# Kernel tuning notes

Measured on AMD Instinct MI355X. Metric: run time of the kernel, lower is better.

## Reference

```python
import math
import numpy as np
import jax, jax.numpy as jnp

LMAX1, LMAX2 = 10, 5
F1, F2 = 20, 40
B_IN, B_L1, B_L2 = 96, 10, 6
ASPECT = 2
BATCH = 32
ACT_CST = math.sqrt(2.0)  # normalize2mom(relu): E[relu(z)^2]=1/2 for z~N(0,1)


def _fact(n):
    return float(math.factorial(n))


def wigner_d_small(l, beta):
    # Wigner small-d matrices, complex-m ordering m=-l..l -> [n, 2l+1, 2l+1]
    beta = np.asarray(beta, dtype=np.float64)
    n = beta.shape[0]
    d = np.zeros((n, 2 * l + 1, 2 * l + 1))
    c, s = np.cos(beta / 2), np.sin(beta / 2)
    for imp, mp in enumerate(range(-l, l + 1)):
        for im, m in enumerate(range(-l, l + 1)):
            pref = math.sqrt(_fact(l + mp) * _fact(l - mp) * _fact(l + m) * _fact(l - m))
            val = np.zeros(n)
            for k in range(max(0, m - mp), min(l + m, l - mp) + 1):
                den = _fact(l + m - k) * _fact(k) * _fact(mp - m + k) * _fact(l - mp - k)
                val += (-1.0) ** (mp - m + k) / den * c ** (2 * l + m - mp - 2 * k) * s ** (mp - m + 2 * k)
            d[:, imp, im] = pref * val
    return d


def U_c2r(l):
    # unitary change of basis complex SH -> real SH, Yr = U @ Yc
    U = np.zeros((2 * l + 1, 2 * l + 1), dtype=np.complex128)
    U[l, l] = 1.0
    sq = 1.0 / math.sqrt(2.0)
    for m in range(1, l + 1):
        cs = (-1.0) ** m
        U[l + m, l + m] = cs * sq
        U[l + m, l - m] = sq
        U[l - m, l + m] = -1j * cs * sq
        U[l - m, l - m] = 1j * sq
    return U


def rot_z_real(l, ang):
    # real-basis rotation about the azimuthal axis -> [n, 2l+1, 2l+1]
    U = U_c2r(l)
    m = np.arange(-l, l + 1)
    ph = np.exp(-1j * np.outer(np.asarray(ang, np.float64), m))
    return np.real(np.einsum('ik,nk,jk->nij', U, ph, U.conj(), optimize=True))


def d_real(l, beta):
    U = U_c2r(l)
    dc = wigner_d_small(l, beta).astype(np.complex128)
    return np.real(np.einsum('ij,njk,lk->nil', U, dc, U.conj(), optimize=True))


def wigner_D_pts(l, a, b, g):
    return np.einsum('nij,njk,nkm->nim', rot_z_real(l, a), d_real(l, b), rot_z_real(l, g), optimize=True)


def flat_wigner_pts(lmax, a, b, g):
    n = len(a)
    return np.concatenate([math.sqrt(2 * l + 1) * wigner_D_pts(l, a, b, g).reshape(n, -1) for l in range(lmax + 1)], -1)


def flat_wigner_grid(lmax, al, be, ga):
    # product grid (alpha x beta x gamma), flattened alpha-major -> [na*nb*ng, sum (2l+1)^2]
    blocks = []
    for l in range(lmax + 1):
        D = np.einsum('aij,bjk,gkm->abgim', rot_z_real(l, al), d_real(l, be), rot_z_real(l, ga), optimize=True)
        blocks.append(math.sqrt(2 * l + 1) * D.reshape(-1, (2 * l + 1) ** 2))
    return np.concatenate(blocks, -1)


def sh_pts(lmax, a, b):
    # component-normalized real SH at points: Y_l = sqrt(2l+1) * D^l(a,b,0)[:, m=0]
    cols = []
    for l in range(lmax + 1):
        M = np.einsum('nij,nj->ni', rot_z_real(l, a), d_real(l, b)[:, :, l], optimize=True)
        cols.append(math.sqrt(2 * l + 1) * M)
    return np.concatenate(cols, -1)


def sh_grid(lmax, al, be):
    # SH on product grid, flattened beta-major to match x.transpose(-1,-2) layout
    cols = []
    for l in range(lmax + 1):
        M = np.einsum('aij,bj->bai', rot_z_real(l, al), d_real(l, be)[:, :, l], optimize=True)
        cols.append(math.sqrt(2 * l + 1) * M.reshape(-1, 2 * l + 1))
    return np.concatenate(cols, -1)


def _so3_grid(res):
    nb, na = 2 * res, 2 * res * ASPECT
    al = 2 * math.pi * np.arange(na) / na
    be = math.pi * (np.arange(nb) + 0.5) / nb
    return al, be, al.copy()


def setup_inputs():
    key = jax.random.key(0)
    k1, k2, k3 = jax.random.split(key, 3)
    # kernel grids (near identity), as in s2/so3_near_identity_grid
    b_s2 = np.arange(1, 4) * (math.pi / 8) / 3
    a_s2 = np.linspace(0, 2 * math.pi, 9)[:-1]
    ga, gb = np.meshgrid(a_s2, b_s2, indexing='ij')
    Yk1 = sh_pts(LMAX1, ga.ravel(), gb.ravel())  # [24, 121]
    a_so3 = np.linspace(0, 2 * math.pi, 8)[:-1]
    g_so3 = np.linspace(-2 * math.pi, 2 * math.pi, 8)
    ga, gb, gg = np.meshgrid(a_so3, b_s2, g_so3, indexing='ij')
    Dk2 = flat_wigner_pts(LMAX2, ga.ravel(), gb.ravel(), gg.ravel())  # [168, 286]
    # FromS2Grid analysis matrix (pinv of band-limited synthesis matrix)
    be = (np.arange(B_IN) + 0.5) / B_IN * math.pi
    al = np.arange(B_IN) / B_IN * 2 * math.pi
    from_s2 = np.linalg.pinv(sh_grid(LMAX1, al, be))  # [121, 9216]
    # SO(3) activation transform matrices
    a1, b1, g1 = _so3_grid(B_L1)
    D1_to = flat_wigner_grid(LMAX1, a1, b1, g1)                     # [32000, 1771]
    F1_from = np.linalg.pinv(flat_wigner_grid(LMAX2, a1, b1, g1))   # [286, 32000]
    a2, b2, g2 = _so3_grid(B_L2)
    D2_to = flat_wigner_grid(LMAX2, a2, b2, g2)                     # [6912, 286]
    F2_from = np.linalg.pinv(flat_wigner_grid(0, a2, b2, g2))       # [1, 6912]
    f32 = lambda v: jnp.asarray(v, dtype=jnp.float32)
    return {
        'x': jax.random.normal(k1, (BATCH, 1, B_IN, B_IN), dtype=jnp.float32),
        'w1': jax.random.normal(k2, (1, F1, Yk1.shape[0]), dtype=jnp.float32),
        'w2': jax.random.normal(k3, (F1, F2, Dk2.shape[0]), dtype=jnp.float32),
        'Yk1': f32(Yk1), 'Dk2': f32(Dk2), 'from_s2': f32(from_s2),
        'D1_to': f32(D1_to), 'F1_from': f32(F1_from),
        'D2_to': f32(D2_to), 'F2_from': f32(F2_from),
    }


def reference(x, w1, w2, Yk1, Dk2, from_s2, D1_to, F1_from, D2_to, F2_from):
    B = x.shape[0]
    # [B,1,alpha,beta] -> [B,1,beta,alpha] -> S2 Fourier coefficients
    c = jnp.einsum('bfg,cg->bfc', jnp.swapaxes(x, -1, -2).reshape(B, 1, -1), from_s2)  # [B,1,121]
    # S2 -> SO(3) convolution (e3nn Linear with SH-built weights)
    psi1 = jnp.einsum('ni,xyn->xyi', Yk1, w1) / math.sqrt(Yk1.shape[0])  # [1,F1,121]
    outs = []
    for l in range(LMAX1 + 1):
        k = 2 * l + 1
        ol = jnp.einsum('bim,ijn->bjnm', c[:, :, l * l:l * l + k], psi1[:, :, l * l:l * l + k])  # fan_in = 1
        outs.append(ol.reshape(B, F1, k * k))
    h = jnp.concatenate(outs, -1)  # [B,F1,1771]
    # SO(3) activation: Fourier -> grid, relu, grid -> Fourier (lmax 10 -> 5)
    g = ACT_CST * jax.nn.relu(jnp.einsum('bfc,gc->bfg', h, D1_to))
    h = jnp.einsum('bfg,cg->bfc', g, F1_from)  # [B,F1,286]
    # SO(3) -> SO(3) convolution (Wigner-D-built weights)
    psi2 = jnp.einsum('nc,xyn->xyc', Dk2, w2) / math.sqrt(Dk2.shape[0])  # [F1,F2,286]
    outs, off = [], 0
    for l in range(LMAX2 + 1):
        k = 2 * l + 1
        xl = h[:, :, off:off + k * k].reshape(B, F1, k, k)       # [B,i,u,m]
        pl = psi2[:, :, off:off + k * k].reshape(F1, F2, k, k)   # [i,j,u,v]
        ol = jnp.einsum('bium,ijuv->bjvm', xl, pl) / math.sqrt(F1 * k)  # fan_in = F1*(2l+1)
        outs.append(ol.reshape(B, F2, k * k))
        off += k * k
    h = jnp.concatenate(outs, -1)  # [B,F2,286]
    # final SO(3) activation lmax 5 -> 0
    g = ACT_CST * jax.nn.relu(jnp.einsum('bfc,gc->bfg', h, D2_to))
    return jnp.einsum('bfg,cg->bfc', g, F2_from)  # [B,F2,1]
```

## Files before the change

kernel.cpp:

```cpp
#include <hip/hip_runtime.h>
#include <hip/hip_bf16.h>
#include <math.h>


#define B_      32
#define F1_     20
#define F2_     40
#define NC1     1771
#define K1P     1792
#define NG1     32000
#define NC2     286
#define K2P     288
#define NG2     6912
#define SQRT2_  1.41421356237309515f
#define RS24    0.20412414523193154f
#define RS168   0.07715167498104595f

typedef unsigned int   uint32;
typedef unsigned short u16;
typedef __attribute__((ext_vector_type(8))) short short8;
typedef __attribute__((ext_vector_type(4))) float f32x4;

#define AS1(p) ((const __attribute__((address_space(1))) void*)(p))
#define AS3(p) ((__attribute__((address_space(3))) void*)(p))

#define WAITCNT_VM4 0x0F74

__device__ __forceinline__ u16 f2bf(float f) {
  uint32 u = __float_as_uint(f);
  return (u16)((u + 0x7FFFu + ((u >> 16) & 1u)) >> 16);
}
__device__ __forceinline__ uint32 pack_bf16(float lo, float hi) {
  uint32 a = __float_as_uint(lo), b = __float_as_uint(hi);
  a = (a + 0x7FFFu + ((a >> 16) & 1u)) >> 16;
  b = (b + 0x7FFFu + ((b >> 16) & 1u)) & 0xFFFF0000u;
  return a | b;
}

__device__ __forceinline__ float wave_reduce(float v) {
#pragma unroll
  for (int o = 32; o > 0; o >>= 1) v += __shfl_down(v, o, 64);
  return v;
}


__global__ void k_xt(const float* __restrict__ x, float* __restrict__ xt) {
  __shared__ float t[32][33];
  const int b = blockIdx.z, i0 = blockIdx.x * 32, j0 = blockIdx.y * 32;
  const int tx = threadIdx.x & 31, ty0 = threadIdx.x >> 5;
  const float* xb = x + b * 9216;
  float* xtb = xt + b * 9216;
#pragma unroll
  for (int r = 0; r < 4; ++r) {
    const int ty = ty0 + r * 8;
    t[ty][tx] = xb[(i0 + ty) * 96 + j0 + tx];
  }
  __syncthreads();
#pragma unroll
  for (int r = 0; r < 4; ++r) {
    const int ty = ty0 + r * 8;
    xtb[(j0 + ty) * 96 + i0 + tx] = t[tx][ty];
  }
}

__global__ void k_c2(const float* __restrict__ xt, const float* __restrict__ fs,
                     float* __restrict__ c) {
  const int ch = blockIdx.x, b = blockIdx.y, tid = threadIdx.x;
  const float4* xb = (const float4*)(xt + b * 9216);
  const float4* fr = (const float4*)(fs + ch * 9216);
  float s = 0.f;
#pragma unroll 3
  for (int g = tid; g < 2304; g += 256) {
    const float4 a = xb[g], d = fr[g];
    s += a.x * d.x + a.y * d.y + a.z * d.z + a.w * d.w;
  }
  s = wave_reduce(s);
  __shared__ float red[4];
  if ((tid & 63) == 0) red[tid >> 6] = s;
  __syncthreads();
  if (tid == 0) c[b * 121 + ch] = red[0] + red[1] + red[2] + red[3];
}

__global__ void k_c(const float* __restrict__ x, const float* __restrict__ fs,
                    float* __restrict__ c) {
  const int ch = blockIdx.x, b = blockIdx.y, tid = threadIdx.x;
  const float* xb = x + b * 9216;
  const float* fr = fs + ch * 9216;
  float s = 0.f;
  for (int g = tid; g < 9216; g += 256) {
    s += xb[(g % 96) * 96 + (g / 96)] * fr[g];
  }
  s = wave_reduce(s);
  __shared__ float red[4];
  if ((tid & 63) == 0) red[tid >> 6] = s;
  __syncthreads();
  if (tid == 0) c[b * 121 + ch] = red[0] + red[1] + red[2] + red[3];
}

__global__ void k_psi1(const float* __restrict__ Yk1, const float* __restrict__ w1,
                       float* __restrict__ psi1) {
  const int j = blockIdx.x, i = threadIdx.x;
  __shared__ float wsm[24];
  if (i < 24) wsm[i] = w1[j * 24 + i];
  __syncthreads();
  if (i < 121) {
    float s = 0.f;
#pragma unroll
    for (int n = 0; n < 24; ++n) s += Yk1[n * 121 + i] * wsm[n];
    psi1[j * 121 + i] = s * RS24;
  }
}

__global__ void k_h(const float* __restrict__ c, const float* __restrict__ psi1,
                    u16* __restrict__ hb) {
  const int j = blockIdx.x, b = blockIdx.y, tid = threadIdx.x;
  __shared__ float cs[121], ps[121];
  if (tid < 121) { cs[tid] = c[b * 121 + tid]; ps[tid] = psi1[j * 121 + tid]; }
  __syncthreads();
  for (int idx = tid; idx < K1P; idx += 256) {
    u16 v = 0;
    if (idx < NC1) {
      int off = 0, l = 0, k = 1;
      while (idx >= off + k * k) { off += k * k; ++l; k += 2; }
      const int r = idx - off, n = r / k, m = r % k;
      v = f2bf(cs[l * l + m] * ps[l * l + n]);
    }
    hb[(size_t)(b * F1_ + j) * K1P + idx] = v;
  }
}


__global__ void k_cvt1(const float* __restrict__ in, uint32* __restrict__ out) {
  const int total = 32000 * 896;
  for (int id = blockIdx.x * 256 + threadIdx.x; id < total; id += gridDim.x * 256) {
    const int r = id / 896, c2 = id % 896, cc = c2 * 2;
    const float* p = in + (size_t)r * NC1 + cc;
    const float lo = (cc < NC1) ? p[0] : 0.f;
    const float hi = (cc + 1 < NC1) ? p[1] : 0.f;
    out[id] = pack_bf16(lo, hi);
  }
}

__global__ void k_cvt2(const float* __restrict__ in, uint32* __restrict__ out) {
  const int total = 286 * 16000;
  for (int id = blockIdx.x * 256 + threadIdx.x; id < total; id += gridDim.x * 256) {
    out[id] = pack_bf16(in[2 * id], in[2 * id + 1]);
  }
}

__global__ void k_cvt3(const float* __restrict__ in, uint32* __restrict__ out) {
  const int total = 6912 * 144;
  for (int id = blockIdx.x * 256 + threadIdx.x; id < total; id += gridDim.x * 256) {
    const int r = id / 144, c2 = id % 144, cc = c2 * 2;
    const float* p = in + (size_t)r * NC2 + cc;
    const float lo = (cc < NC2) ? p[0] : 0.f;
    const float hi = (cc + 1 < NC2) ? p[1] : 0.f;
    out[id] = pack_bf16(lo, hi);
  }
}


__launch_bounds__(256)
__global__ void k_gemm1_v4(const u16* __restrict__ A, const u16* __restrict__ B,
                           u16* __restrict__ C) {
  __shared__ __align__(16) u16 As0[128 * 32], As1[128 * 32], As2[128 * 32];
  __shared__ __align__(16) u16 Bs0[128 * 32], Bs1[128 * 32], Bs2[128 * 32];
  const int bid = blockIdx.x;
  const int gg = bid / 40, loc = bid % 40;
  int nt, mt;
  if (gg < 31) { nt = gg * 8 + (loc & 7); mt = loc >> 3; }
  else         { nt = 248 + (loc & 1);   mt = loc >> 1; }
  const int m0 = mt * 128, n0 = nt * 128;
  const int tid = threadIdx.x;
  const int lane = tid & 63, w = tid >> 6;
  const int wm = w >> 1, wn = w & 1;
  const int q = lane >> 4, r16 = lane & 15;

  const u16* ag = A + (size_t)(m0 + (tid >> 2)) * K1P + (tid & 3) * 8;
  const u16* bg = B + (size_t)(n0 + (tid >> 2)) * K1P + (tid & 3) * 8;

#define G1_ISSUE(kk, Asb, Bsb)                                                   \
  {                                                                              \
    _Pragma("unroll")                                                            \
    for (int i = 0; i < 2; ++i) {                                                \
      __builtin_amdgcn_global_load_lds(AS1(ag + (kk) * 32 + (size_t)i * 64 * K1P), \
          AS3((char*)(Asb) + i * 4096 + w * 1024), 16, 0, 0);                    \
      __builtin_amdgcn_global_load_lds(AS1(bg + (kk) * 32 + (size_t)i * 64 * K1P), \
          AS3((char*)(Bsb) + i * 4096 + w * 1024), 16, 0, 0);                    \
    }                                                                            \
  }

#define G1_COMPUTE(Asb, Bsb)                                                     \
  {                                                                              \
    short8 af[4], bq[4];                                                         \
    _Pragma("unroll")                                                            \
    for (int mb = 0; mb < 4; ++mb)                                               \
      af[mb] = *(const short8*)&(Asb)[(wm * 64 + mb * 16 + r16) * 32 + q * 8];   \
    _Pragma("unroll")                                                            \
    for (int nb = 0; nb < 4; ++nb)                                               \
      bq[nb] = *(const short8*)&(Bsb)[(wn * 64 + nb * 16 + r16) * 32 + q * 8];   \
    _Pragma("unroll")                                                            \
    for (int mb = 0; mb < 4; ++mb)                                               \
      _Pragma("unroll")                                                          \
      for (int nb = 0; nb < 4; ++nb)                                             \
        acc[mb][nb] = __builtin_amdgcn_mfma_f32_16x16x32_bf16(af[mb], bq[nb],    \
                                                              acc[mb][nb], 0, 0, 0); \
  }

#define G1_STAGE(kk, AsR, BsR, AsI, BsI)        \
  {                                             \
    __builtin_amdgcn_s_waitcnt(WAITCNT_VM4);    \
    __builtin_amdgcn_s_barrier();               \
    asm volatile("" ::: "memory");              \
    if ((kk) + 2 < 56) G1_ISSUE((kk) + 2, AsI, BsI) \
    G1_COMPUTE(AsR, BsR)                        \
  }

  f32x4 acc[4][4] = {};
  G1_ISSUE(0, As0, Bs0)
  G1_ISSUE(1, As1, Bs1)
  for (int k = 0; k < 54; k += 3) {
    G1_STAGE(k,     As0, Bs0, As2, Bs2)
    G1_STAGE(k + 1, As1, Bs1, As0, Bs0)
    G1_STAGE(k + 2, As2, Bs2, As1, Bs1)
  }
  G1_STAGE(54, As0, Bs0, As2, Bs2)
  G1_STAGE(55, As1, Bs1, As0, Bs0)

#pragma unroll
  for (int mb = 0; mb < 4; ++mb) {
#pragma unroll
    for (int nb = 0; nb < 4; ++nb) {
      const int col = n0 + wn * 64 + nb * 16 + r16;
#pragma unroll
      for (int r = 0; r < 4; ++r) {
        const int row = m0 + wm * 64 + mb * 16 + q * 4 + r;
        float v = acc[mb][nb][r];
        v = (v > 0.f) ? v * SQRT2_ : 0.f;
        C[(size_t)row * NG1 + col] = f2bf(v);
      }
    }
  }
#undef G1_ISSUE
#undef G1_COMPUTE
#undef G1_STAGE
}

__launch_bounds__(256)
__global__ void k_gemm2_v4(const u16* __restrict__ A, const u16* __restrict__ B,
                           float* __restrict__ C) {
  __shared__ __align__(16) u16 As0[128 * 32], As1[128 * 32], As2[128 * 32];
  __shared__ __align__(16) u16 Bs0[128 * 32], Bs1[128 * 32], Bs2[128 * 32];
  const int m0 = blockIdx.x * 128, n0 = blockIdx.y * 128;
  const int ks = blockIdx.z * 1600;
  const int tid = threadIdx.x;
  const int lane = tid & 63, w = tid >> 6;
  const int wm = w >> 1, wn = w & 1;
  const int q = lane >> 4, r16 = lane & 15;

  const u16* ag = A + (size_t)(m0 + (tid >> 2)) * NG1 + ks + (tid & 3) * 8;
  int rb0 = n0 + (tid >> 2);        if (rb0 > 285) rb0 = 285;
  int rb1 = n0 + (tid >> 2) + 64;   if (rb1 > 285) rb1 = 285;
  const u16* bg0 = B + (size_t)rb0 * NG1 + ks + (tid & 3) * 8;
  const u16* bg1 = B + (size_t)rb1 * NG1 + ks + (tid & 3) * 8;

#define G2_ISSUE(kk, Asb, Bsb)                                                   \
  {                                                                              \
    _Pragma("unroll")                                                            \
    for (int i = 0; i < 2; ++i)                                                  \
      __builtin_amdgcn_global_load_lds(AS1(ag + (kk) * 32 + (size_t)i * 64 * NG1), \
          AS3((char*)(Asb) + i * 4096 + w * 1024), 16, 0, 0);                    \
    __builtin_amdgcn_global_load_lds(AS1(bg0 + (kk) * 32),                       \
        AS3((char*)(Bsb) + w * 1024), 16, 0, 0);                                 \
    __builtin_amdgcn_global_load_lds(AS1(bg1 + (kk) * 32),                       \
        AS3((char*)(Bsb) + 4096 + w * 1024), 16, 0, 0);                          \
  }

#define G2_COMPUTE(Asb, Bsb)                                                     \
  {                                                                              \
    short8 af[4], bq[4];                                                         \
    _Pragma("unroll")                                                            \
    for (int mb = 0; mb < 4; ++mb)                                               \
      af[mb] = *(const short8*)&(Asb)[(wm * 64 + mb * 16 + r16) * 32 + q * 8];   \
    _Pragma("unroll")                                                            \
    for (int nb = 0; nb < 4; ++nb)                                               \
      bq[nb] = *(const short8*)&(Bsb)[(wn * 64 + nb * 16 + r16) * 32 + q * 8];   \
    _Pragma("unroll")                                                            \
    for (int mb = 0; mb < 4; ++mb)                                               \
      _Pragma("unroll")                                                          \
      for (int nb = 0; nb < 4; ++nb)                                             \
        acc[mb][nb] = __builtin_amdgcn_mfma_f32_16x16x32_bf16(af[mb], bq[nb],    \
                                                              acc[mb][nb], 0, 0, 0); \
  }

#define G2_STAGE(kk, AsR, BsR, AsI, BsI)        \
  {                                             \
    __builtin_amdgcn_s_waitcnt(WAITCNT_VM4);    \
    __builtin_amdgcn_s_barrier();               \
    asm volatile("" ::: "memory");              \
    if ((kk) + 2 < 50) G2_ISSUE((kk) + 2, AsI, BsI) \
    G2_COMPUTE(AsR, BsR)                        \
  }

  f32x4 acc[4][4] = {};
  G2_ISSUE(0, As0, Bs0)
  G2_ISSUE(1, As1, Bs1)
  for (int k = 0; k < 48; k += 3) {
    G2_STAGE(k,     As0, Bs0, As2, Bs2)
    G2_STAGE(k + 1, As1, Bs1, As0, Bs0)
    G2_STAGE(k + 2, As2, Bs2, As1, Bs1)
  }
  G2_STAGE(48, As0, Bs0, As2, Bs2)
  G2_STAGE(49, As1, Bs1, As0, Bs0)

#pragma unroll
  for (int mb = 0; mb < 4; ++mb) {
#pragma unroll
    for (int nb = 0; nb < 4; ++nb) {
      const int col = n0 + wn * 64 + nb * 16 + r16;
      if (col < NC2) {
#pragma unroll
        for (int r = 0; r < 4; ++r) {
          const int row = m0 + wm * 64 + mb * 16 + q * 4 + r;
          atomicAdd(&C[(size_t)row * NC2 + col], acc[mb][nb][r]);
        }
      }
    }
  }
#undef G2_ISSUE
#undef G2_COMPUTE
#undef G2_STAGE
}

__launch_bounds__(256)
__global__ void k_gemm3_v3(const u16* __restrict__ A, const u16* __restrict__ B,
                           const float* __restrict__ wv, float* __restrict__ out) {
  __shared__ __align__(16) u16 As[128 * 32];
  __shared__ __align__(16) u16 Bs[128 * 32];
  __shared__ float red[128][33];
  const int m0 = blockIdx.x * 128, n0 = blockIdx.y * 128;
  const int tid = threadIdx.x;
  const int lane = tid & 63, w = tid >> 6;
  const int wm = w >> 1, wn = w & 1;
  const int q = lane >> 4, r16 = lane & 15;

  f32x4 acc[4][4] = {};
  const u16* ag = A + (size_t)(m0 + (tid >> 2)) * K2P + (tid & 3) * 8;
  const u16* bg = B + (size_t)(n0 + (tid >> 2)) * K2P + (tid & 3) * 8;

  for (int k0 = 0; k0 < K2P; k0 += 32) {
#pragma unroll
    for (int i = 0; i < 2; ++i) {
      __builtin_amdgcn_global_load_lds(AS1(ag + k0 + (size_t)i * 64 * K2P),
                                       AS3((char*)As + i * 4096 + w * 1024), 16, 0, 0);
      __builtin_amdgcn_global_load_lds(AS1(bg + k0 + (size_t)i * 64 * K2P),
                                       AS3((char*)Bs + i * 4096 + w * 1024), 16, 0, 0);
    }
    __syncthreads();
    short8 af[4], bq[4];
#pragma unroll
    for (int mb = 0; mb < 4; ++mb)
      af[mb] = *(const short8*)&As[(wm * 64 + mb * 16 + r16) * 32 + q * 8];
#pragma unroll
    for (int nb = 0; nb < 4; ++nb)
      bq[nb] = *(const short8*)&Bs[(wn * 64 + nb * 16 + r16) * 32 + q * 8];
#pragma unroll
    for (int mb = 0; mb < 4; ++mb)
#pragma unroll
      for (int nb = 0; nb < 4; ++nb)
        acc[mb][nb] = __builtin_amdgcn_mfma_f32_16x16x32_bf16(af[mb], bq[nb], acc[mb][nb], 0, 0, 0);
    __syncthreads();
  }
  float wvv[4];
#pragma unroll
  for (int nb = 0; nb < 4; ++nb) wvv[nb] = wv[n0 + wn * 64 + nb * 16 + r16];
#pragma unroll
  for (int mb = 0; mb < 4; ++mb) {
#pragma unroll
    for (int r = 0; r < 4; ++r) {
      const int rowl = wm * 64 + mb * 16 + q * 4 + r;
      float t = 0.f;
#pragma unroll
      for (int nb = 0; nb < 4; ++nb) {
        float v = acc[mb][nb][r];
        v = (v > 0.f) ? v : 0.f;
        t += v * wvv[nb];
      }
      red[rowl][wn * 16 + r16] = t;
    }
  }
  __syncthreads();
  if (tid < 128) {
    float s = 0.f;
#pragma unroll
    for (int cc = 0; cc < 32; ++cc) s += red[tid][cc];
    atomicAdd(&out[m0 + tid], s * SQRT2_);
  }
}


__launch_bounds__(256)
__global__ void k_gemm1_mfma(const u16* __restrict__ A, const float* __restrict__ Bf,
                             u16* __restrict__ C) {
  __shared__ __align__(16) u16 As[128 * 32];
  __shared__ __align__(16) u16 Bs[128 * 32];
  const int tid = threadIdx.x;
  const int lane = tid & 63, w = tid >> 6;
  const int wm = w >> 1, wn = w & 1;
  const int q = lane >> 4, r16 = lane & 15;
  const int m0 = blockIdx.x * 128, n0 = blockIdx.y * 128;

  f32x4 acc[4][4] = {};
  const u16* ag = A + (size_t)(m0 + (tid >> 2)) * K1P + (tid & 3) * 8;

  for (int k0 = 0; k0 < K1P; k0 += 32) {
#pragma unroll
    for (int i = 0; i < 2; ++i) {
      __builtin_amdgcn_global_load_lds(AS1(ag + k0 + (size_t)i * 64 * K1P),
                                       AS3((char*)As + i * 4096 + w * 1024), 16, 0, 0);
    }
#pragma unroll
    for (int i = 0; i < 8; ++i) {
      const int p = i * 256 + tid;
      const int row = p >> 4, c2 = (p & 15) * 2;
      const int kk = k0 + c2;
      const float* bp = Bf + (size_t)(n0 + row) * NC1 + kk;
      const float lo = (kk < NC1) ? bp[0] : 0.f;
      const float hi = (kk + 1 < NC1) ? bp[1] : 0.f;
      ((uint32*)Bs)[row * 16 + (p & 15)] = pack_bf16(lo, hi);
    }
    __syncthreads();
    short8 af[4], bq[4];
#pragma unroll
    for (int mb = 0; mb < 4; ++mb)
      af[mb] = *(const short8*)&As[(wm * 64 + mb * 16 + r16) * 32 + q * 8];
#pragma unroll
    for (int nb = 0; nb < 4; ++nb)
      bq[nb] = *(const short8*)&Bs[(wn * 64 + nb * 16 + r16) * 32 + q * 8];
#pragma unroll
    for (int mb = 0; mb < 4; ++mb)
#pragma unroll
      for (int nb = 0; nb < 4; ++nb)
        acc[mb][nb] = __builtin_amdgcn_mfma_f32_16x16x32_bf16(af[mb], bq[nb], acc[mb][nb], 0, 0, 0);
    __syncthreads();
  }
#pragma unroll
  for (int mb = 0; mb < 4; ++mb) {
#pragma unroll
    for (int nb = 0; nb < 4; ++nb) {
      const int col = n0 + wn * 64 + nb * 16 + r16;
#pragma unroll
      for (int r = 0; r < 4; ++r) {
        const int row = m0 + wm * 64 + mb * 16 + q * 4 + r;
        float v = acc[mb][nb][r];
        v = (v > 0.f) ? v * SQRT2_ : 0.f;
        C[(size_t)row * NG1 + col] = f2bf(v);
      }
    }
  }
}

__launch_bounds__(256)
__global__ void k_gemm2_mfma(const u16* __restrict__ A, const float* __restrict__ Bf,
                             float* __restrict__ C) {
  __shared__ __align__(16) u16 As[128 * 32];
  __shared__ __align__(16) u16 Bs[128 * 32];
  const int tid = threadIdx.x;
  const int lane = tid & 63, w = tid >> 6;
  const int wm = w >> 1, wn = w & 1;
  const int q = lane >> 4, r16 = lane & 15;
  const int m0 = blockIdx.x * 128, n0 = blockIdx.y * 128;
  const int ks = blockIdx.z * 1600;

  f32x4 acc[4][4] = {};
  const u16* ag = A + (size_t)(m0 + (tid >> 2)) * NG1 + ks + (tid & 3) * 8;

  for (int kt = 0; kt < 1600; kt += 32) {
#pragma unroll
    for (int i = 0; i < 2; ++i) {
      __builtin_amdgcn_global_load_lds(AS1(ag + kt + (size_t)i * 64 * NG1),
                                       AS3((char*)As + i * 4096 + w * 1024), 16, 0, 0);
    }
#pragma unroll
    for (int i = 0; i < 4; ++i) {
      const int idx = i * 256 + tid;
      const int row = idx >> 3, c4 = (idx & 7) * 4;
      const int n = n0 + row;
      float4 v = make_float4(0.f, 0.f, 0.f, 0.f);
      if (n < NC2) v = *(const float4*)(Bf + (size_t)n * NG1 + ks + kt + c4);
      ((uint32*)Bs)[row * 16 + (idx & 7) * 2]     = pack_bf16(v.x, v.y);
      ((uint32*)Bs)[row * 16 + (idx & 7) * 2 + 1] = pack_bf16(v.z, v.w);
    }
    __syncthreads();
    short8 af[4], bq[4];
#pragma unroll
    for (int mb = 0; mb < 4; ++mb)
      af[mb] = *(const short8*)&As[(wm * 64 + mb * 16 + r16) * 32 + q * 8];
#pragma unroll
    for (int nb = 0; nb < 4; ++nb)
      bq[nb] = *(const short8*)&Bs[(wn * 64 + nb * 16 + r16) * 32 + q * 8];
#pragma unroll
    for (int mb = 0; mb < 4; ++mb)
#pragma unroll
      for (int nb = 0; nb < 4; ++nb)
        acc[mb][nb] = __builtin_amdgcn_mfma_f32_16x16x32_bf16(af[mb], bq[nb], acc[mb][nb], 0, 0, 0);
    __syncthreads();
  }
#pragma unroll
  for (int mb = 0; mb < 4; ++mb) {
#pragma unroll
    for (int nb = 0; nb < 4; ++nb) {
      const int col = n0 + wn * 64 + nb * 16 + r16;
      if (col < NC2) {
#pragma unroll
        for (int r = 0; r < 4; ++r) {
          const int row = m0 + wm * 64 + mb * 16 + q * 4 + r;
          atomicAdd(&C[(size_t)row * NC2 + col], acc[mb][nb][r]);
        }
      }
    }
  }
}


__global__ void k_psi2(const float* __restrict__ Dk2, const float* __restrict__ w2,
                       float* __restrict__ psi2) {
  const int blk = blockIdx.x, tid = threadIdx.x;
  __shared__ float w2s[168];
  if (tid < 168) w2s[tid] = w2[blk * 168 + tid];
  __syncthreads();
  for (int cc = tid; cc < NC2; cc += 256) {
    float s = 0.f;
    for (int n = 0; n < 168; ++n) s += Dk2[n * NC2 + cc] * w2s[n];
    psi2[blk * NC2 + cc] = s * RS168;
  }
}

__global__ void k_step7(const float* __restrict__ h2, const float* __restrict__ psi2,
                        u16* __restrict__ h3b) {
  const int j = blockIdx.x, b = blockIdx.y, tid = threadIdx.x;
  __shared__ float sh[20 * 286];
  __shared__ float sp[20 * 286];
  for (int e = tid; e < 20 * 286; e += 256) {
    const int i = e / 286, cc = e % 286;
    sh[e] = h2[(b * F1_ + i) * NC2 + cc];
    sp[e] = psi2[(i * F2_ + j) * NC2 + cc];
  }
  __syncthreads();
  for (int cidx = tid; cidx < K2P; cidx += 256) {
    u16 ov = 0;
    if (cidx < NC2) {
      int off = 0, l = 0, k = 1;
      while (cidx >= off + k * k) { off += k * k; ++l; k += 2; }
      const int r = cidx - off, v = r / k, m = r % k;
      float acc = 0.f;
      for (int i = 0; i < 20; ++i) {
        const float* hbp = &sh[i * 286 + off];
        const float* pb = &sp[i * 286 + off];
        for (int u = 0; u < k; ++u) acc += hbp[u * k + m] * pb[u * k + v];
      }
      ov = f2bf(acc * rsqrtf(20.f * (float)k));
    }
    h3b[(size_t)(b * F2_ + j) * K2P + cidx] = ov;
  }
}


extern "C" void kernel_launch(void* const* d_in, const int* in_sizes, int n_in,
                              void* d_out, int out_size, void* d_ws, size_t ws_size,
                              hipStream_t stream) {
  const float* x       = (const float*)d_in[0];
  const float* w1      = (const float*)d_in[1];
  const float* w2      = (const float*)d_in[2];
  const float* Yk1     = (const float*)d_in[3];
  const float* Dk2     = (const float*)d_in[4];
  const float* from_s2 = (const float*)d_in[5];
  const float* D1_to   = (const float*)d_in[6];
  const float* F1_from = (const float*)d_in[7];
  const float* D2_to   = (const float*)d_in[8];
  const float* F2_from = (const float*)d_in[9];
  float* out = (float*)d_out;

  float* ws = (float*)d_ws;
  float* c    = ws + 0;
  float* psi1 = ws + 3872;
  float* h2   = ws + 6292;
  float* psi2 = ws + 189332;
  u16*   h3b  = (u16*)(ws + 418132);
  u16*   hb   = (u16*)(ws + 602452);
  u16*   g    = (u16*)(ws + 1175892);
  u16*   D2bf = (u16*)(ws + 11415892);
  u16*   F1bf = (u16*)(ws + 12411220);
  u16*   D1bf = (u16*)(ws + 16987220);
  float* x_t  = ws + 45659220;
  const size_t BIG_NEED = (size_t)45659220 * 4;
  const size_t XT_NEED  = (size_t)45954132 * 4;
  const bool big   = ws_size >= BIG_NEED;
  const bool useXT = ws_size >= XT_NEED;

  if (useXT) {
    k_xt<<<dim3(3, 3, 32), 256, 0, stream>>>(x, x_t);
    k_c2<<<dim3(121, 32),  256, 0, stream>>>(x_t, from_s2, c);
  } else {
    k_c <<<dim3(121, 32),  256, 0, stream>>>(x, from_s2, c);
  }
  k_psi1<<<dim3(20),      128, 0, stream>>>(Yk1, w1, psi1);
  k_h   <<<dim3(20, 32),  256, 0, stream>>>(c, psi1, hb);
  k_cvt3<<<dim3(1024),    256, 0, stream>>>(D2_to, (uint32*)D2bf);

  if (big) {
    k_cvt1<<<dim3(8192), 256, 0, stream>>>(D1_to, (uint32*)D1bf);
    k_cvt2<<<dim3(4096), 256, 0, stream>>>(F1_from, (uint32*)F1bf);
    k_gemm1_v4<<<dim3(1250), 256, 0, stream>>>(hb, D1bf, g);
    hipMemsetAsync(h2, 0, (size_t)640 * 286 * sizeof(float), stream);
    k_gemm2_v4<<<dim3(5, 3, 20), 256, 0, stream>>>(g, F1bf, h2);
  } else {
    k_gemm1_mfma<<<dim3(5, 250), 256, 0, stream>>>(hb, D1_to, g);
    hipMemsetAsync(h2, 0, (size_t)640 * 286 * sizeof(float), stream);
    k_gemm2_mfma<<<dim3(5, 3, 20), 256, 0, stream>>>(g, F1_from, h2);
  }

  k_psi2 <<<dim3(800),    256, 0, stream>>>(Dk2, w2, psi2);
  k_step7<<<dim3(40, 32), 256, 0, stream>>>(h2, psi2, h3b);

  hipMemsetAsync(out, 0, (size_t)1280 * sizeof(float), stream);
  k_gemm3_v3<<<dim3(10, 54), 256, 0, stream>>>(h3b, D2bf, F2_from, out);
}
```

Measured before the change: 674.8 us.

## Replace LDS-staged GEMM pipelines with direct global-to-register double-buffered MFMA loads

Both large GEMM kernels drop the three-stage LDS ring buffer filled by global_load_lds with barriers. Each wave now loads its MFMA operand fragments straight from global memory into registers, double-buffered across k-chunks, with launch bounds requesting 3 blocks per CU. GEMM2's split-K changes from 20 to 25 slices of 1280. This removes LDS traffic and block-wide barriers but gives up cross-wave reuse through shared memory, so each wave refetches A/B rows from global/L2 with 16-byte strided accesses, raising cache pressure.

```diff
diff --git a/kernel.cpp b/kernel.cpp
--- a/kernel.cpp
+++ b/kernel.cpp
@@ -24,8 +24,6 @@
 #define AS1(p) ((const __attribute__((address_space(1))) void*)(p))
 #define AS3(p) ((__attribute__((address_space(3))) void*)(p))
 
-#define WAITCNT_VM4 0x0F74
-
 __device__ __forceinline__ u16 f2bf(float f) {
   uint32 u = __float_as_uint(f);
   return (u16)((u + 0x7FFFu + ((u >> 16) & 1u)) >> 16);
@@ -160,11 +158,27 @@
 }
 
 
-__launch_bounds__(256)
-__global__ void k_gemm1_v4(const u16* __restrict__ A, const u16* __restrict__ B,
+#define MFMA16(ab, bb)                                                          \
+  {                                                                             \
+    _Pragma("unroll")                                                           \
+    for (int mb = 0; mb < 4; ++mb)                                              \
+      _Pragma("unroll")                                                         \
+      for (int nb = 0; nb < 4; ++nb)                                            \
+        acc[mb][nb] = __builtin_amdgcn_mfma_f32_16x16x32_bf16((ab)[mb], (bb)[nb], \
+                                                              acc[mb][nb], 0, 0, 0); \
+  }
+
+#define LD8(ab, bb, kc)                                                         \
+  {                                                                             \
+    _Pragma("unroll")                                                           \
+    for (int mb = 0; mb < 4; ++mb) (ab)[mb] = *(const short8*)(ap[mb] + (kc) * 32); \
+    _Pragma("unroll")                                                           \
+    for (int nb = 0; nb < 4; ++nb) (bb)[nb] = *(const short8*)(bp[nb] + (kc) * 32); \
+  }
+
+__launch_bounds__(256, 3)
+__global__ void k_gemm1_v5(const u16* __restrict__ A, const u16* __restrict__ B,
                            u16* __restrict__ C) {
-  __shared__ __align__(16) u16 As0[128 * 32], As1[128 * 32], As2[128 * 32];
-  __shared__ __align__(16) u16 Bs0[128 * 32], Bs1[128 * 32], Bs2[128 * 32];
   const int bid = blockIdx.x;
   const int gg = bid / 40, loc = bid % 40;
   int nt, mt;
@@ -176,56 +190,27 @@
   const int wm = w >> 1, wn = w & 1;
   const int q = lane >> 4, r16 = lane & 15;
 
-  const u16* ag = A + (size_t)(m0 + (tid >> 2)) * K1P + (tid & 3) * 8;
-  const u16* bg = B + (size_t)(n0 + (tid >> 2)) * K1P + (tid & 3) * 8;
-
-#define G1_ISSUE(kk, Asb, Bsb)                                                   \
-  {                                                                              \
-    _Pragma("unroll")                                                            \
-    for (int i = 0; i < 2; ++i) {                                                \
-      __builtin_amdgcn_global_load_lds(AS1(ag + (kk) * 32 + (size_t)i * 64 * K1P), \
-          AS3((char*)(Asb) + i * 4096 + w * 1024), 16, 0, 0);                    \
-      __builtin_amdgcn_global_load_lds(AS1(bg + (kk) * 32 + (size_t)i * 64 * K1P), \
-          AS3((char*)(Bsb) + i * 4096 + w * 1024), 16, 0, 0);                    \
-    }                                                                            \
-  }
-
-#define G1_COMPUTE(Asb, Bsb)                                                     \
-  {                                                                              \
-    short8 af[4], bq[4];                                                         \
-    _Pragma("unroll")                                                            \
-    for (int mb = 0; mb < 4; ++mb)                                               \
-      af[mb] = *(const short8*)&(Asb)[(wm * 64 + mb * 16 + r16) * 32 + q * 8];   \
-    _Pragma("unroll")                                                            \
-    for (int nb = 0; nb < 4; ++nb)                                               \
-      bq[nb] = *(const short8*)&(Bsb)[(wn * 64 + nb * 16 + r16) * 32 + q * 8];   \
-    _Pragma("unroll")                                                            \
-    for (int mb = 0; mb < 4; ++mb)                                               \
-      _Pragma("unroll")                                                          \
-      for (int nb = 0; nb < 4; ++nb)                                             \
-        acc[mb][nb] = __builtin_amdgcn_mfma_f32_16x16x32_bf16(af[mb], bq[nb],    \
-                                                              acc[mb][nb], 0, 0, 0); \
-  }
-
-#define G1_STAGE(kk, AsR, BsR, AsI, BsI)        \
-  {                                             \
-    __builtin_amdgcn_s_waitcnt(WAITCNT_VM4);    \
-    __builtin_amdgcn_s_barrier();               \
-    asm volatile("" ::: "memory");              \
-    if ((kk) + 2 < 56) G1_ISSUE((kk) + 2, AsI, BsI) \
-    G1_COMPUTE(AsR, BsR)                        \
-  }
+  const u16* ap[4];
+  const u16* bp[4];
+#pragma unroll
+  for (int mb = 0; mb < 4; ++mb)
+    ap[mb] = A + (size_t)(m0 + wm * 64 + mb * 16 + r16) * K1P + q * 8;
+#pragma unroll
+  for (int nb = 0; nb < 4; ++nb)
+    bp[nb] = B + (size_t)(n0 + wn * 64 + nb * 16 + r16) * K1P + q * 8;
 
   f32x4 acc[4][4] = {};
-  G1_ISSUE(0, As0, Bs0)
-  G1_ISSUE(1, As1, Bs1)
-  for (int k = 0; k < 54; k += 3) {
-    G1_STAGE(k,     As0, Bs0, As2, Bs2)
-    G1_STAGE(k + 1, As1, Bs1, As0, Bs0)
-    G1_STAGE(k + 2, As2, Bs2, As1, Bs1)
-  }
-  G1_STAGE(54, As0, Bs0, As2, Bs2)
-  G1_STAGE(55, As1, Bs1, As0, Bs0)
+  short8 a0[4], b0[4], a1[4], b1[4];
+  LD8(a0, b0, 0)
+  LD8(a1, b1, 1)
+  for (int kc = 0; kc < 54; kc += 2) {
+    MFMA16(a0, b0)
+    LD8(a0, b0, kc + 2)
+    MFMA16(a1, b1)
+    LD8(a1, b1, kc + 3)
+  }
+  MFMA16(a0, b0)
+  MFMA16(a1, b1)
 
 #pragma unroll
   for (int mb = 0; mb < 4; ++mb) {
@@ -241,77 +226,42 @@
       }
     }
   }
-#undef G1_ISSUE
-#undef G1_COMPUTE
-#undef G1_STAGE
-}
-
-__launch_bounds__(256)
-__global__ void k_gemm2_v4(const u16* __restrict__ A, const u16* __restrict__ B,
+}
+
+__launch_bounds__(256, 3)
+__global__ void k_gemm2_v5(const u16* __restrict__ A, const u16* __restrict__ B,
                            float* __restrict__ C) {
-  __shared__ __align__(16) u16 As0[128 * 32], As1[128 * 32], As2[128 * 32];
-  __shared__ __align__(16) u16 Bs0[128 * 32], Bs1[128 * 32], Bs2[128 * 32];
   const int m0 = blockIdx.x * 128, n0 = blockIdx.y * 128;
-  const int ks = blockIdx.z * 1600;
+  const int ksc = blockIdx.z * 40;
   const int tid = threadIdx.x;
   const int lane = tid & 63, w = tid >> 6;
   const int wm = w >> 1, wn = w & 1;
   const int q = lane >> 4, r16 = lane & 15;
 
-  const u16* ag = A + (size_t)(m0 + (tid >> 2)) * NG1 + ks + (tid & 3) * 8;
-  int rb0 = n0 + (tid >> 2);        if (rb0 > 285) rb0 = 285;
-  int rb1 = n0 + (tid >> 2) + 64;   if (rb1 > 285) rb1 = 285;
-  const u16* bg0 = B + (size_t)rb0 * NG1 + ks + (tid & 3) * 8;
-  const u16* bg1 = B + (size_t)rb1 * NG1 + ks + (tid & 3) * 8;
-
-#define G2_ISSUE(kk, Asb, Bsb)                                                   \
-  {                                                                              \
-    _Pragma("unroll")                                                            \
-    for (int i = 0; i < 2; ++i)                                                  \
-      __builtin_amdgcn_global_load_lds(AS1(ag + (kk) * 32 + (size_t)i * 64 * NG1), \
-          AS3((char*)(Asb) + i * 4096 + w * 1024), 16, 0, 0);                    \
-    __builtin_amdgcn_global_load_lds(AS1(bg0 + (kk) * 32),                       \
-        AS3((char*)(Bsb) + w * 1024), 16, 0, 0);                                 \
-    __builtin_amdgcn_global_load_lds(AS1(bg1 + (kk) * 32),                       \
-        AS3((char*)(Bsb) + 4096 + w * 1024), 16, 0, 0);                          \
-  }
-
-#define G2_COMPUTE(Asb, Bsb)                                                     \
-  {                                                                              \
-    short8 af[4], bq[4];                                                         \
-    _Pragma("unroll")                                                            \
-    for (int mb = 0; mb < 4; ++mb)                                               \
-      af[mb] = *(const short8*)&(Asb)[(wm * 64 + mb * 16 + r16) * 32 + q * 8];   \
-    _Pragma("unroll")                                                            \
-    for (int nb = 0; nb < 4; ++nb)                                               \
-      bq[nb] = *(const short8*)&(Bsb)[(wn * 64 + nb * 16 + r16) * 32 + q * 8];   \
-    _Pragma("unroll")                                                            \
-    for (int mb = 0; mb < 4; ++mb)                                               \
-      _Pragma("unroll")                                                          \
-      for (int nb = 0; nb < 4; ++nb)                                             \
-        acc[mb][nb] = __builtin_amdgcn_mfma_f32_16x16x32_bf16(af[mb], bq[nb],    \
-                                                              acc[mb][nb], 0, 0, 0); \
-  }
-
-#define G2_STAGE(kk, AsR, BsR, AsI, BsI)        \
-  {                                             \
-    __builtin_amdgcn_s_waitcnt(WAITCNT_VM4);    \
-    __builtin_amdgcn_s_barrier();               \
-    asm volatile("" ::: "memory");              \
-    if ((kk) + 2 < 50) G2_ISSUE((kk) + 2, AsI, BsI) \
-    G2_COMPUTE(AsR, BsR)                        \
+  const u16* ap[4];
+  const u16* bp[4];
+#pragma unroll
+  for (int mb = 0; mb < 4; ++mb)
+    ap[mb] = A + (size_t)(m0 + wm * 64 + mb * 16 + r16) * NG1 + (size_t)ksc * 32 + q * 8;
+#pragma unroll
+  for (int nb = 0; nb < 4; ++nb) {
+    int rr = n0 + wn * 64 + nb * 16 + r16;
+    if (rr > 285) rr = 285;
+    bp[nb] = B + (size_t)rr * NG1 + (size_t)ksc * 32 + q * 8;
   }
 
   f32x4 acc[4][4] = {};
-  G2_ISSUE(0, As0, Bs0)
-  G2_ISSUE(1, As1, Bs1)
-  for (int k = 0; k < 48; k += 3) {
-    G2_STAGE(k,     As0, Bs0, As2, Bs2)
-    G2_STAGE(k + 1, As1, Bs1, As0, Bs0)
-    G2_STAGE(k + 2, As2, Bs2, As1, Bs1)
-  }
-  G2_STAGE(48, As0, Bs0, As2, Bs2)
-  G2_STAGE(49, As1, Bs1, As0, Bs0)
+  short8 a0[4], b0[4], a1[4], b1[4];
+  LD8(a0, b0, 0)
+  LD8(a1, b1, 1)
+  for (int kc = 0; kc < 38; kc += 2) {
+    MFMA16(a0, b0)
+    LD8(a0, b0, kc + 2)
+    MFMA16(a1, b1)
+    LD8(a1, b1, kc + 3)
+  }
+  MFMA16(a0, b0)
+  MFMA16(a1, b1)
 
 #pragma unroll
   for (int mb = 0; mb < 4; ++mb) {
@@ -327,9 +277,6 @@
       }
     }
   }
-#undef G2_ISSUE
-#undef G2_COMPUTE
-#undef G2_STAGE
 }
 
 __launch_bounds__(256)
@@ -424,9 +371,9 @@
       const int p = i * 256 + tid;
       const int row = p >> 4, c2 = (p & 15) * 2;
       const int kk = k0 + c2;
-      const float* bp = Bf + (size_t)(n0 + row) * NC1 + kk;
-      const float lo = (kk < NC1) ? bp[0] : 0.f;
-      const float hi = (kk + 1 < NC1) ? bp[1] : 0.f;
+      const float* bpp = Bf + (size_t)(n0 + row) * NC1 + kk;
+      const float lo = (kk < NC1) ? bpp[0] : 0.f;
+      const float hi = (kk + 1 < NC1) ? bpp[1] : 0.f;
       ((uint32*)Bs)[row * 16 + (p & 15)] = pack_bf16(lo, hi);
     }
     __syncthreads();
@@ -611,9 +558,9 @@
   if (big) {
     k_cvt1<<<dim3(8192), 256, 0, stream>>>(D1_to, (uint32*)D1bf);
     k_cvt2<<<dim3(4096), 256, 0, stream>>>(F1_from, (uint32*)F1bf);
-    k_gemm1_v4<<<dim3(1250), 256, 0, stream>>>(hb, D1bf, g);
+    k_gemm1_v5<<<dim3(1250), 256, 0, stream>>>(hb, D1bf, g);
     hipMemsetAsync(h2, 0, (size_t)640 * 286 * sizeof(float), stream);
-    k_gemm2_v4<<<dim3(5, 3, 20), 256, 0, stream>>>(g, F1bf, h2);
+    k_gemm2_v5<<<dim3(5, 3, 25), 256, 0, stream>>>(g, F1bf, h2);
   } else {
     k_gemm1_mfma<<<dim3(5, 250), 256, 0, stream>>>(hb, D1_to, g);
     hipMemsetAsync(h2, 0, (size_t)640 * 286 * sizeof(float), stream);
```

Result: slower. 842.8 us (+24.9%).
